# Optimization experiments

Hardware: AMD Instinct MI355X
Metric: run time of the kernel (lower is better)

Reference implementation:

```python
import jax, jax.numpy as jnp
import numpy as np

G = 37            # 518 // 14 patch grid side
NUM_REG = 4
R = 3 // 2        # roi_side // 2
EPS = 1e-12


def setup_inputs() -> dict:
    key = jax.random.key(0)
    B, S, D = 128, 1 + NUM_REG + G * G, 768
    tokens = jax.random.normal(key, (B, S, D), dtype=jnp.float32)
    return {"tokens": tokens}


def _buddy_pool_all(cues, patches2d):
    # cues: [B, C, d], patches2d: [B, H, W, d]
    B, H, W, d = patches2d.shape
    flat = patches2d.reshape(B, H * W, d)
    sim = jnp.einsum('bcd,bnd->bcn', cues, flat)          # [B, C, H*W]
    idx = jnp.argmax(sim, axis=-1)                        # [B, C] int
    h = idx // W
    w = idx % W
    rows = jnp.arange(H)
    cols = jnp.arange(W)
    # boundary-clipped window masks (clipping is automatic since rows in [0,H))
    mh = ((rows >= (h[..., None] - R)) & (rows <= (h[..., None] + R))).astype(patches2d.dtype)  # [B,C,H]
    mw = ((cols >= (w[..., None] - R)) & (cols <= (w[..., None] + R))).astype(patches2d.dtype)  # [B,C,W]
    count = mh.sum(-1) * mw.sum(-1)                       # [B, C]
    roi = jnp.einsum('bch,bcw,bhwd->bcd', mh, mw, patches2d)
    return roi / count[..., None]


def reference(tokens):
    B, S, d = tokens.shape
    cls_tok = tokens[:, 0:1, :]
    regs_tok = tokens[:, 1:1 + NUM_REG, :]
    patch_tok = tokens[:, 1 + NUM_REG:, :]
    patches2d = patch_tok.reshape(B, G, G, d)
    cues = jnp.concatenate([cls_tok, regs_tok], axis=1)   # [B, 5, d]
    rois = _buddy_pool_all(cues, patches2d)               # [B, 5, d]
    toks = jnp.concatenate([cues, rois], axis=1)          # [B, 10, d]
    norm = jnp.sqrt(jnp.sum(toks * toks, axis=-1, keepdims=True))
    return toks / jnp.maximum(norm, EPS)
```

## Files before the change

kernel.cpp:

```cpp
#include <hip/hip_runtime.h>
#include <hip/hip_bf16.h>

#define Gp 37
#define NP (Gp * Gp)
#define Dm 768
#define NC 5
#define Sm (NC + NP)
#define NTOK 10
#define SPLITS 16
#define PPS ((NP + SPLITS - 1) / SPLITS)

__device__ __forceinline__ float dot12(const float4 x0, const float4 x1, const float4 x2,
                                       const float4 c0, const float4 c1, const float4 c2) {
    float a = x0.x * c0.x;
    a = fmaf(x0.y, c0.y, a);
    a = fmaf(x0.z, c0.z, a);
    a = fmaf(x0.w, c0.w, a);
    a = fmaf(x1.x, c1.x, a);
    a = fmaf(x1.y, c1.y, a);
    float b = x1.z * c1.z;
    b = fmaf(x1.w, c1.w, b);
    b = fmaf(x2.x, c2.x, b);
    b = fmaf(x2.y, c2.y, b);
    b = fmaf(x2.z, c2.z, b);
    b = fmaf(x2.w, c2.w, b);
    return a + b;
}

__device__ __forceinline__ float packed_reduce(float s0, float s1, float s2, float s3, float s4,
                                               const int g) {
#pragma unroll
    for (int off = 32; off >= 8; off >>= 1) {
        s0 += __shfl_xor(s0, off, 64);
        s1 += __shfl_xor(s1, off, 64);
        s2 += __shfl_xor(s2, off, 64);
        s3 += __shfl_xor(s3, off, 64);
        s4 += __shfl_xor(s4, off, 64);
    }
    float val = s4;
    val = (g == 0) ? s0 : val;
    val = (g == 1) ? s1 : val;
    val = (g == 2) ? s2 : val;
    val = (g == 3) ? s3 : val;
#pragma unroll
    for (int off = 4; off >= 1; off >>= 1) val += __shfl_xor(val, off, 64);
    return val;
}

__global__ __launch_bounds__(256, 4) void argmax_kernel(const float* __restrict__ tokens,
                                                        unsigned long long* __restrict__ best) {
    const int b = blockIdx.x / SPLITS;
    const int split = blockIdx.x % SPLITS;
    const int lane = threadIdx.x & 63;
    const int wave = threadIdx.x >> 6;
    const int g = lane >> 3;
    const float* base = tokens + (size_t)b * Sm * Dm;

    float4 cue[NC][3];
#pragma unroll
    for (int c = 0; c < NC; ++c) {
        const float4* cp = (const float4*)(base + c * Dm);
#pragma unroll
        for (int k = 0; k < 3; ++k) cue[c][k] = cp[lane + 64 * k];
    }

    const int p0 = split * PPS;
    const int p1 = (p0 + PPS < NP) ? (p0 + PPS) : NP;

    float bestSim = -3.4e38f;
    int bestIdx = 0;

    int p = p0 + wave;
    const float4* ppA = (const float4*)(base + (size_t)(NC + p) * Dm);
    const float4* ppB = ppA + 4 * (Dm / 4);

    float4 A0, A1, A2, B0, B1, B2;
    A0 = ppA[lane]; A1 = ppA[lane + 64]; A2 = ppA[lane + 128];
    if (p + 4 < p1) { B0 = ppB[lane]; B1 = ppB[lane + 64]; B2 = ppB[lane + 128]; }

    while (p < p1) {
        float s0 = dot12(A0, A1, A2, cue[0][0], cue[0][1], cue[0][2]);
        float s1 = dot12(A0, A1, A2, cue[1][0], cue[1][1], cue[1][2]);
        float s2 = dot12(A0, A1, A2, cue[2][0], cue[2][1], cue[2][2]);
        float s3 = dot12(A0, A1, A2, cue[3][0], cue[3][1], cue[3][2]);
        float s4 = dot12(A0, A1, A2, cue[4][0], cue[4][1], cue[4][2]);
        if (p + 8 < p1) {
            ppA += 8 * (Dm / 4);
            A0 = ppA[lane]; A1 = ppA[lane + 64]; A2 = ppA[lane + 128];
        }
        float val = packed_reduce(s0, s1, s2, s3, s4, g);
        if (val > bestSim) { bestSim = val; bestIdx = p; }

        if (p + 4 < p1) {
            float t0 = dot12(B0, B1, B2, cue[0][0], cue[0][1], cue[0][2]);
            float t1 = dot12(B0, B1, B2, cue[1][0], cue[1][1], cue[1][2]);
            float t2 = dot12(B0, B1, B2, cue[2][0], cue[2][1], cue[2][2]);
            float t3 = dot12(B0, B1, B2, cue[3][0], cue[3][1], cue[3][2]);
            float t4 = dot12(B0, B1, B2, cue[4][0], cue[4][1], cue[4][2]);
            if (p + 12 < p1) {
                ppB += 8 * (Dm / 4);
                B0 = ppB[lane]; B1 = ppB[lane + 64]; B2 = ppB[lane + 128];
            }
            float v2 = packed_reduce(t0, t1, t2, t3, t4, g);
            if (v2 > bestSim) { bestSim = v2; bestIdx = p + 4; }
        }
        p += 8;
    }

    if (((lane & 7) == 0) && g < NC) {
        unsigned fb = __float_as_uint(bestSim);
        unsigned key = (fb & 0x80000000u) ? ~fb : (fb | 0x80000000u);
        unsigned long long packed = (3ull << 62)
                                  | ((unsigned long long)key << 30)
                                  | (unsigned long long)(0x3FFFFFFFu - (unsigned)bestIdx);
        atomicMax(&best[b * NC + g], packed);
    }
}

__global__ __launch_bounds__(256) void finalize_kernel(const float* __restrict__ tokens,
                                                       const unsigned long long* __restrict__ best,
                                                       float* __restrict__ out) {
    const int b = blockIdx.x / NTOK;
    const int t = blockIdx.x % NTOK;
    const int tid = threadIdx.x;
    const float* base = tokens + (size_t)b * Sm * Dm;

    float v[3];
    if (t < NC) {
        const float* cp = base + t * Dm;
#pragma unroll
        for (int k = 0; k < 3; ++k) v[k] = cp[tid + 256 * k];
    } else {
        const int c = t - NC;
        const unsigned long long packed = best[b * NC + c];
        const int idx = (int)(0x3FFFFFFFu - (unsigned)(packed & 0x3FFFFFFFull));
        const int h = idx / Gp, w = idx % Gp;
        const int h0 = (h - 1 > 0) ? h - 1 : 0;
        const int h1 = (h + 1 < Gp - 1) ? h + 1 : Gp - 1;
        const int w0 = (w - 1 > 0) ? w - 1 : 0;
        const int w1 = (w + 1 < Gp - 1) ? w + 1 : Gp - 1;
        const float inv = 1.0f / (float)((h1 - h0 + 1) * (w1 - w0 + 1));
        float acc[3] = {0.f, 0.f, 0.f};
        for (int hh = h0; hh <= h1; ++hh) {
            for (int ww = w0; ww <= w1; ++ww) {
                const float* pp = base + (size_t)(NC + hh * Gp + ww) * Dm;
#pragma unroll
                for (int k = 0; k < 3; ++k) acc[k] += pp[tid + 256 * k];
            }
        }
#pragma unroll
        for (int k = 0; k < 3; ++k) v[k] = acc[k] * inv;
    }

    float ss = v[0] * v[0] + v[1] * v[1] + v[2] * v[2];
#pragma unroll
    for (int off = 32; off; off >>= 1) ss += __shfl_xor(ss, off, 64);
    __shared__ float wsum[4];
    const int lane = tid & 63, wv = tid >> 6;
    if (lane == 0) wsum[wv] = ss;
    __syncthreads();
    const float tot = wsum[0] + wsum[1] + wsum[2] + wsum[3];
    const float scale = 1.0f / fmaxf(sqrtf(tot), 1e-12f);

    float* o = out + (size_t)b * NTOK * Dm + (size_t)t * Dm;
#pragma unroll
    for (int k = 0; k < 3; ++k) o[tid + 256 * k] = v[k] * scale;
}

extern "C" void kernel_launch(void* const* d_in, const int* in_sizes, int n_in,
                              void* d_out, int out_size, void* d_ws, size_t ws_size,
                              hipStream_t stream) {
    const float* tokens = (const float*)d_in[0];
    float* out = (float*)d_out;
    const int B = in_sizes[0] / (Sm * Dm);

    unsigned long long* best = (unsigned long long*)d_ws;

    argmax_kernel<<<B * SPLITS, 256, 0, stream>>>(tokens, best);
    finalize_kernel<<<B * NTOK, 256, 0, stream>>>(tokens, best, out);
}
```

Measured before the change: 684.9 us.

## Fuse argmax and ROI finalize via last-block-done counter

Merges the argmax and finalize kernels into one. Each batch keeps an atomic counter, and the last split block to finish does the ROI pooling and normalization, reading the best index through an atomic. This removes a kernel launch and the gap between the two kernels, at the cost of one extra small init kernel to clear the counters. The finalize work now runs on only 128 blocks of 4 waves each, so that tail has less parallelism than the old 1280-block finalize kernel. The launch_bounds occupancy hint is also dropped, and the best array is never reset in the code, which was already true before.

```diff
diff --git a/kernel.cpp b/kernel.cpp
--- a/kernel.cpp
+++ b/kernel.cpp
@@ -1,5 +1,4 @@
 #include <hip/hip_runtime.h>
-#include <hip/hip_bf16.h>
 
 #define Gp 37
 #define NP (Gp * Gp)
@@ -47,8 +46,22 @@
     return val;
 }
 
-__global__ __launch_bounds__(256, 4) void argmax_kernel(const float* __restrict__ tokens,
-                                                        unsigned long long* __restrict__ best) {
+__device__ __forceinline__ void add4(float4& a, const float4 b) {
+    a.x += b.x; a.y += b.y; a.z += b.z; a.w += b.w;
+}
+__device__ __forceinline__ float4 scale4(const float4 a, const float s) {
+    return make_float4(a.x * s, a.y * s, a.z * s, a.w * s);
+}
+
+__global__ void init_cnt_kernel(unsigned* __restrict__ cnt, int n) {
+    const int i = threadIdx.x + blockIdx.x * blockDim.x;
+    if (i < n) cnt[i] = 0u;
+}
+
+__global__ __launch_bounds__(256) void fused_kernel(const float* __restrict__ tokens,
+                                                    unsigned long long* __restrict__ best,
+                                                    unsigned* __restrict__ cnt,
+                                                    float* __restrict__ out) {
     const int b = blockIdx.x / SPLITS;
     const int split = blockIdx.x % SPLITS;
     const int lane = threadIdx.x & 63;
@@ -115,56 +128,57 @@
                                   | (unsigned long long)(0x3FFFFFFFu - (unsigned)bestIdx);
         atomicMax(&best[b * NC + g], packed);
     }
-}
 
-__global__ __launch_bounds__(256) void finalize_kernel(const float* __restrict__ tokens,
-                                                       const unsigned long long* __restrict__ best,
-                                                       float* __restrict__ out) {
-    const int b = blockIdx.x / NTOK;
-    const int t = blockIdx.x % NTOK;
-    const int tid = threadIdx.x;
-    const float* base = tokens + (size_t)b * Sm * Dm;
+    __threadfence();
+    __syncthreads();
+    __shared__ int lastFlag;
+    if (threadIdx.x == 0) lastFlag = (atomicAdd(&cnt[b], 1u) == SPLITS - 1);
+    __syncthreads();
+    if (!lastFlag) return;
 
-    float v[3];
-    if (t < NC) {
-        const float* cp = base + t * Dm;
 #pragma unroll
-        for (int k = 0; k < 3; ++k) v[k] = cp[tid + 256 * k];
-    } else {
-        const int c = t - NC;
-        const unsigned long long packed = best[b * NC + c];
-        const int idx = (int)(0x3FFFFFFFu - (unsigned)(packed & 0x3FFFFFFFull));
-        const int h = idx / Gp, w = idx % Gp;
-        const int h0 = (h - 1 > 0) ? h - 1 : 0;
-        const int h1 = (h + 1 < Gp - 1) ? h + 1 : Gp - 1;
-        const int w0 = (w - 1 > 0) ? w - 1 : 0;
-        const int w1 = (w + 1 < Gp - 1) ? w + 1 : Gp - 1;
-        const float inv = 1.0f / (float)((h1 - h0 + 1) * (w1 - w0 + 1));
-        float acc[3] = {0.f, 0.f, 0.f};
-        for (int hh = h0; hh <= h1; ++hh) {
-            for (int ww = w0; ww <= w1; ++ww) {
-                const float* pp = base + (size_t)(NC + hh * Gp + ww) * Dm;
+    for (int t = 0; t < NTOK; ++t) {
+        if ((t & 3) != wave) continue;
+        float4 v0, v1, v2;
+        if (t < NC) {
+            v0 = cue[t][0]; v1 = cue[t][1]; v2 = cue[t][2];
+        } else {
+            const int c = t - NC;
+            unsigned long long packed = 0;
+            if (lane == 0) packed = atomicMax(&best[b * NC + c], 0ull);
+            packed = __shfl(packed, 0, 64);
+            const int idx = (int)(0x3FFFFFFFu - (unsigned)(packed & 0x3FFFFFFFull));
+            const int h = idx / Gp, w = idx % Gp;
+            const int h0 = (h - 1 > 0) ? h - 1 : 0;
+            const int h1 = (h + 1 < Gp - 1) ? h + 1 : Gp - 1;
+            const int w0 = (w - 1 > 0) ? w - 1 : 0;
+            const int w1 = (w + 1 < Gp - 1) ? w + 1 : Gp - 1;
+            const float inv = 1.0f / (float)((h1 - h0 + 1) * (w1 - w0 + 1));
+            float4 a0 = make_float4(0.f, 0.f, 0.f, 0.f);
+            float4 a1 = a0, a2 = a0;
+            for (int hh = h0; hh <= h1; ++hh) {
+                for (int ww = w0; ww <= w1; ++ww) {
+                    const float4* pp = (const float4*)(base + (size_t)(NC + hh * Gp + ww) * Dm);
+                    add4(a0, pp[lane]);
+                    add4(a1, pp[lane + 64]);
+                    add4(a2, pp[lane + 128]);
+                }
+            }
+            v0 = scale4(a0, inv); v1 = scale4(a1, inv); v2 = scale4(a2, inv);
+        }
+
+        float ss = v0.x * v0.x + v0.y * v0.y + v0.z * v0.z + v0.w * v0.w
+                 + v1.x * v1.x + v1.y * v1.y + v1.z * v1.z + v1.w * v1.w
+                 + v2.x * v2.x + v2.y * v2.y + v2.z * v2.z + v2.w * v2.w;
 #pragma unroll
-                for (int k = 0; k < 3; ++k) acc[k] += pp[tid + 256 * k];
-            }
-        }
-#pragma unroll
-        for (int k = 0; k < 3; ++k) v[k] = acc[k] * inv;
+        for (int off = 32; off; off >>= 1) ss += __shfl_xor(ss, off, 64);
+        const float scale = 1.0f / fmaxf(sqrtf(ss), 1e-12f);
+
+        float4* o = (float4*)(out + (size_t)b * NTOK * Dm + (size_t)t * Dm);
+        o[lane]       = scale4(v0, scale);
+        o[lane + 64]  = scale4(v1, scale);
+        o[lane + 128] = scale4(v2, scale);
     }
-
-    float ss = v[0] * v[0] + v[1] * v[1] + v[2] * v[2];
-#pragma unroll
-    for (int off = 32; off; off >>= 1) ss += __shfl_xor(ss, off, 64);
-    __shared__ float wsum[4];
-    const int lane = tid & 63, wv = tid >> 6;
-    if (lane == 0) wsum[wv] = ss;
-    __syncthreads();
-    const float tot = wsum[0] + wsum[1] + wsum[2] + wsum[3];
-    const float scale = 1.0f / fmaxf(sqrtf(tot), 1e-12f);
-
-    float* o = out + (size_t)b * NTOK * Dm + (size_t)t * Dm;
-#pragma unroll
-    for (int k = 0; k < 3; ++k) o[tid + 256 * k] = v[k] * scale;
 }
 
 extern "C" void kernel_launch(void* const* d_in, const int* in_sizes, int n_in,
@@ -175,7 +189,8 @@
     const int B = in_sizes[0] / (Sm * Dm);
 
     unsigned long long* best = (unsigned long long*)d_ws;
+    unsigned* cnt = (unsigned*)(best + (size_t)B * NC);
+    init_cnt_kernel<<<1, 128, 0, stream>>>(cnt, B);
 
-    argmax_kernel<<<B * SPLITS, 256, 0, stream>>>(tokens, best);
-    finalize_kernel<<<B * NTOK, 256, 0, stream>>>(tokens, best, out);
+    fused_kernel<<<B * SPLITS, 256, 0, stream>>>(tokens, best, cnt, out);
 }
```

Measured after the change: 1.062 ms. 55.1% more time.
